# Performance work log

Measured on AMD Instinct MI355X. Metric: run time of the kernel, lower is better.

The kernel has to match this reference:

```python
import jax, jax.numpy as jnp
import numpy as np

N = 20000      # cells (nodes)
E = 640000     # kNN edges (before self loops)
IN = 2000      # gene features
C = 64         # out_channels
H = 4          # attention heads
NEG_SLOPE = 0.2
EPS = 1e-12


def setup_inputs() -> dict:
    key = jax.random.key(0)
    ks = jax.random.split(key, 12)
    s = lambda k, shape, sc: (jax.random.normal(k, shape, jnp.float32) * sc)
    x = s(ks[0], (N, IN), 1.0)
    edge_index = jax.random.randint(ks[1], (2, E), 0, N)
    W_ae = s(ks[2], (IN, C), 0.02); b_ae = jnp.zeros((C,), jnp.float32)
    Wl = s(ks[3], (C, H * C), 0.1); bl = jnp.zeros((H * C,), jnp.float32)
    Wr = s(ks[4], (C, H * C), 0.1); br = jnp.zeros((H * C,), jnp.float32)
    att = s(ks[5], (H, C), 0.1)
    b_conv = jnp.zeros((H * C,), jnp.float32)
    W_lin = s(ks[6], (H * C, C), 0.1); b_lin = jnp.zeros((C,), jnp.float32)
    ln_w = jnp.ones((C,), jnp.float32); ln_b = jnp.zeros((C,), jnp.float32)
    return dict(x=x, edge_index=edge_index, W_ae=W_ae, b_ae=b_ae, Wl=Wl, bl=bl,
                Wr=Wr, br=br, att=att, b_conv=b_conv, W_lin=W_lin, b_lin=b_lin,
                ln_w=ln_w, ln_b=ln_b)


def reference(x, edge_index, W_ae, b_ae, Wl, bl, Wr, br, att, b_conv,
              W_lin, b_lin, ln_w, ln_b):
    # Encoder.AE: linear projection of gene features -> node embeddings
    h = x @ W_ae + b_ae                              # [N, C]

    # GATv2Conv (PyG defaults: add_self_loops=True, negative_slope=0.2,
    # dropout is identity at eval, concat=True)
    loops = jnp.arange(N)
    src = jnp.concatenate([edge_index[0], loops])    # [E+N] message sources j
    dst = jnp.concatenate([edge_index[1], loops])    # [E+N] targets i

    xl = (h @ Wl + bl).reshape(N, H, C)              # W_l x (source features)
    xr = (h @ Wr + br).reshape(N, H, C)              # W_r x (target features)

    g = jax.nn.leaky_relu(xl[src] + xr[dst], NEG_SLOPE)   # [E+N, H, C]
    logits = jnp.einsum('ehc,hc->eh', g, att)             # [E+N, H]

    # segment softmax over incoming edges of each target node
    m = jax.ops.segment_max(logits, dst, num_segments=N)  # [N, H]
    e = jnp.exp(logits - m[dst])
    denom = jax.ops.segment_sum(e, dst, num_segments=N)   # [N, H] (>0: self loops)
    alpha = e / denom[dst]                                 # [E+N, H]

    out = jax.ops.segment_sum(alpha[:, :, None] * xl[src], dst, num_segments=N)
    out = out.reshape(N, H * C) + b_conv             # concat heads + bias

    # Encoder.linear + activation (relu), dropout = identity at eval
    a = jax.nn.relu(out @ W_lin + b_lin)             # [N, C]

    # residual + TF-style LayerNorm
    y = a + h
    u = y.mean(-1, keepdims=True)
    v = ((y - u) ** 2).mean(-1, keepdims=True)
    return ln_w * (y - u) / jnp.sqrt(v + EPS) + ln_b
```

## Files before the change

kernel.cpp:

```cpp
#include <hip/hip_runtime.h>
#include <hip/hip_fp16.h>

#define N_NODES 20000
#define N_EDGES 640000
#define IN_F    2000
#define KPAD    2048
#define C_OUT   64
#define HC      256
#define NEG     0.2f
#define SCAN_B  79

typedef __attribute__((ext_vector_type(4))) float f32x4;
typedef __attribute__((ext_vector_type(8))) short bf16x8;
typedef _Float16 h2 __attribute__((ext_vector_type(2)));

__device__ inline unsigned short f2bf(float f) {
    unsigned u = __float_as_uint(f);
    return (unsigned short)((u + 0x7FFFu + ((u >> 16) & 1u)) >> 16);
}


__global__ void k_hist(const int* __restrict__ dst, int* __restrict__ counts) {
    int e = blockIdx.x * blockDim.x + threadIdx.x;
    if (e < N_EDGES) atomicAdd(&counts[dst[e]], 1);
}

__global__ void k_scan1(const int* __restrict__ counts, int* __restrict__ bsum) {
    int t = threadIdx.x, b = blockIdx.x;
    int i = b * 256 + t;
    int v = (i < N_NODES) ? counts[i] : 0;
    int s = v;
    #pragma unroll
    for (int d = 1; d < 64; d <<= 1) s += __shfl_xor(s, d, 64);
    __shared__ int ws[4];
    if ((t & 63) == 0) ws[t >> 6] = s;
    __syncthreads();
    if (t == 0) bsum[b] = ws[0] + ws[1] + ws[2] + ws[3];
}

__global__ void k_scan2(const int* __restrict__ bsum, int* __restrict__ bbase,
                        int* __restrict__ offsets) {
    int lane = threadIdx.x;
    int v0 = (lane < SCAN_B) ? bsum[lane] : 0;
    int v1 = (64 + lane < SCAN_B) ? bsum[64 + lane] : 0;
    int s0 = v0;
    #pragma unroll
    for (int d = 1; d < 64; d <<= 1) { int t = __shfl_up(s0, d, 64); if (lane >= d) s0 += t; }
    int tot0 = __shfl(s0, 63, 64);
    int s1 = v1;
    #pragma unroll
    for (int d = 1; d < 64; d <<= 1) { int t = __shfl_up(s1, d, 64); if (lane >= d) s1 += t; }
    int tot1 = __shfl(s1, 63, 64);
    if (lane < SCAN_B) bbase[lane] = s0 - v0;
    if (64 + lane < SCAN_B) bbase[64 + lane] = tot0 + s1 - v1;
    if (lane == 0) offsets[N_NODES] = tot0 + tot1;
}

__global__ void k_scan3(const int* __restrict__ counts, const int* __restrict__ bbase,
                        int* __restrict__ offsets, int* __restrict__ cursor) {
    int t = threadIdx.x, b = blockIdx.x;
    int lane = t & 63, wid = t >> 6;
    int i = b * 256 + t;
    int v = (i < N_NODES) ? counts[i] : 0;
    int s = v;
    #pragma unroll
    for (int d = 1; d < 64; d <<= 1) { int u = __shfl_up(s, d, 64); if (lane >= d) s += u; }
    __shared__ int ws[4];
    if (lane == 63) ws[wid] = s;
    __syncthreads();
    int wb = 0;
    #pragma unroll
    for (int w = 0; w < 3; ++w) if (w < wid) wb += ws[w];
    int excl = bbase[b] + wb + (s - v);
    if (i < N_NODES) { offsets[i] = excl; cursor[i] = excl; }
}

__global__ void k_scatter(const int* __restrict__ src, const int* __restrict__ dst,
                          int* __restrict__ cursor, int* __restrict__ ssrc) {
    int e = blockIdx.x * blockDim.x + threadIdx.x;
    if (e < N_EDGES) {
        int d = dst[e];
        int p = atomicAdd(&cursor[d], 1);
        ssrc[p] = src[e];
    }
}


__global__ void k_wt(const float* __restrict__ W, unsigned short* __restrict__ Wt) {
    int idx = blockIdx.x * 256 + threadIdx.x;
    int n = idx >> 11;
    int k = idx & 2047;
    float v = (k < IN_F) ? W[(size_t)k * C_OUT + n] : 0.f;
    Wt[(size_t)n * KPAD + k] = f2bf(v);
}


__global__ __launch_bounds__(256) void k_gemm_h(
    const float* __restrict__ x, const unsigned short* __restrict__ Wt,
    const float* __restrict__ b, float* __restrict__ h) {
    __shared__ unsigned short Asw[32 * 64];
    __shared__ unsigned short Bsw[64 * 64];
    int t = threadIdx.x;
    int lane = t & 63, wid = t >> 6;
    int wr = wid >> 1, wc = wid & 1;
    int row0 = blockIdx.x * 32;

    int a_row = t & 31, a_half = t >> 5;
    int b_n = t >> 2, b_kq = t & 3;

    int rA = wr * 16 + (lane & 15);
    int kchunk = lane >> 4;
    f32x4 acc0 = {0.f, 0.f, 0.f, 0.f}, acc1 = {0.f, 0.f, 0.f, 0.f};

    for (int k0 = 0; k0 < KPAD; k0 += 64) {
        {
            uint4 wv = {0u, 0u, 0u, 0u};
            int kbase = k0 + a_half * 8;
            if (kbase < IN_F) {
                const float* src = &x[(size_t)(row0 + a_row) * IN_F + kbase];
                float4 f0 = *(const float4*)src;
                float4 f1 = *(const float4*)(src + 4);
                wv.x = (unsigned)f2bf(f0.x) | ((unsigned)f2bf(f0.y) << 16);
                wv.y = (unsigned)f2bf(f0.z) | ((unsigned)f2bf(f0.w) << 16);
                wv.z = (unsigned)f2bf(f1.x) | ((unsigned)f2bf(f1.y) << 16);
                wv.w = (unsigned)f2bf(f1.z) | ((unsigned)f2bf(f1.w) << 16);
            }
            int slot = a_half ^ (a_row & 7);
            *(uint4*)((char*)Asw + a_row * 128 + slot * 16) = wv;
        }
        {
            const uint4* src = (const uint4*)&Wt[(size_t)b_n * KPAD + k0 + b_kq * 16];
            uint4 w0 = src[0], w1 = src[1];
            int s0 = (b_kq * 2) ^ (b_n & 7);
            int s1 = (b_kq * 2 + 1) ^ (b_n & 7);
            *(uint4*)((char*)Bsw + b_n * 128 + s0 * 16) = w0;
            *(uint4*)((char*)Bsw + b_n * 128 + s1 * 16) = w1;
        }
        __syncthreads();
        #pragma unroll
        for (int ks = 0; ks < 2; ++ks) {
            int aslot = (ks * 4 + kchunk) ^ (rA & 7);
            bf16x8 af = *(bf16x8*)((char*)Asw + rA * 128 + aslot * 16);
            {
                int cb = wc * 32 + (lane & 15);
                int bslot = (ks * 4 + kchunk) ^ (cb & 7);
                bf16x8 bfr = *(bf16x8*)((char*)Bsw + cb * 128 + bslot * 16);
                acc0 = __builtin_amdgcn_mfma_f32_16x16x32_bf16(af, bfr, acc0, 0, 0, 0);
            }
            {
                int cb = wc * 32 + 16 + (lane & 15);
                int bslot = (ks * 4 + kchunk) ^ (cb & 7);
                bf16x8 bfr = *(bf16x8*)((char*)Bsw + cb * 128 + bslot * 16);
                acc1 = __builtin_amdgcn_mfma_f32_16x16x32_bf16(af, bfr, acc1, 0, 0, 0);
            }
        }
        __syncthreads();
    }
    int ci = (lane >> 4) * 4;
    int cj = lane & 15;
    #pragma unroll
    for (int nt = 0; nt < 2; ++nt) {
        f32x4 a = nt ? acc1 : acc0;
        int col = wc * 32 + nt * 16 + cj;
        float bb = b[col];
        #pragma unroll
        for (int r = 0; r < 4; ++r) {
            int grow = row0 + wr * 16 + ci + r;
            h[(size_t)grow * C_OUT + col] = a[r] + bb;
        }
    }
}


__global__ __launch_bounds__(256) void k_xlxr2(
    const float* __restrict__ h, const float* __restrict__ Wl, const float* __restrict__ bl,
    const float* __restrict__ Wr, const float* __restrict__ br,
    unsigned short* __restrict__ xlh, float* __restrict__ xr) {
    __shared__ float hs[64][68];
    __shared__ float Ws[64][128];
    int t = threadIdx.x;
    int mb = blockIdx.x >> 2, nb = blockIdx.x & 3;
    int node0 = mb * 64;
    const float* Wsrc = (nb < 2) ? (Wl + nb * 128) : (Wr + (nb - 2) * 128);
    const float* bsrc = (nb < 2) ? (bl + nb * 128) : (br + (nb - 2) * 128);

    {
        int row = t >> 2, q = t & 3;
        int gnode = node0 + row; if (gnode >= N_NODES) gnode = N_NODES - 1;
        const float4* src = (const float4*)&h[(size_t)gnode * C_OUT + q * 16];
        *(float4*)&hs[row][q * 16 + 0]  = src[0];
        *(float4*)&hs[row][q * 16 + 4]  = src[1];
        *(float4*)&hs[row][q * 16 + 8]  = src[2];
        *(float4*)&hs[row][q * 16 + 12] = src[3];
    }
    {
        #pragma unroll
        for (int i = 0; i < 8; ++i) {
            int f = t + i * 256;
            int k = f >> 5, c4 = (f & 31) << 2;
            *(float4*)&Ws[k][c4] = *(const float4*)&Wsrc[(size_t)k * HC + c4];
        }
    }
    __syncthreads();

    int tr = t >> 5;
    int tc = t & 31;
    float4 acc[8];
    float4 bv = *(const float4*)&bsrc[tc * 4];
    #pragma unroll
    for (int r = 0; r < 8; ++r) acc[r] = bv;

    for (int k4 = 0; k4 < 64; k4 += 4) {
        float4 w0 = *(float4*)&Ws[k4 + 0][tc * 4];
        float4 w1 = *(float4*)&Ws[k4 + 1][tc * 4];
        float4 w2 = *(float4*)&Ws[k4 + 2][tc * 4];
        float4 w3 = *(float4*)&Ws[k4 + 3][tc * 4];
        #pragma unroll
        for (int r = 0; r < 8; ++r) {
            float4 a = *(float4*)&hs[tr * 8 + r][k4];
            acc[r].x += a.x * w0.x + a.y * w1.x + a.z * w2.x + a.w * w3.x;
            acc[r].y += a.x * w0.y + a.y * w1.y + a.z * w2.y + a.w * w3.y;
            acc[r].z += a.x * w0.z + a.y * w1.z + a.z * w2.z + a.w * w3.z;
            acc[r].w += a.x * w0.w + a.y * w1.w + a.z * w2.w + a.w * w3.w;
        }
    }
    #pragma unroll
    for (int r = 0; r < 8; ++r) {
        int gnode = node0 + tr * 8 + r;
        if (gnode < N_NODES) {
            if (nb < 2) {
                h2 lo = { (_Float16)acc[r].x, (_Float16)acc[r].y };
                h2 hi = { (_Float16)acc[r].z, (_Float16)acc[r].w };
                uint2 o = { __builtin_bit_cast(unsigned, lo),
                            __builtin_bit_cast(unsigned, hi) };
                *(uint2*)&xlh[(size_t)gnode * HC + nb * 128 + tc * 4] = o;
            } else {
                *(float4*)&xr[(size_t)gnode * HC + (nb - 2) * 128 + tc * 4] = acc[r];
            }
        }
    }
}


__global__ __launch_bounds__(256) void k_attn(
    const unsigned short* __restrict__ xlh, const float* __restrict__ xr,
    const float* __restrict__ h, const int* __restrict__ offsets,
    const int* __restrict__ ssrc, const float* __restrict__ att,
    const float* __restrict__ b_conv, const float* __restrict__ W_lin,
    const float* __restrict__ b_lin, const float* __restrict__ ln_w,
    const float* __restrict__ ln_b, float* __restrict__ out) {
    __shared__ float sh[4][HC];
    int wid = threadIdx.x >> 6, lane = threadIdx.x & 63;
    int node = blockIdx.x * 4 + wid;
    int sub = lane >> 4;
    int sl  = lane & 15;
    int c0  = sl * 16;

    const h2 z2  = { (_Float16)0.f, (_Float16)0.f };
    const h2 ns2 = { (_Float16)NEG, (_Float16)NEG };

    h2 xr2[8], at2[8];
    #pragma unroll
    for (int i = 0; i < 4; ++i) {
        float4 t4 = *(const float4*)&xr[(size_t)node * HC + c0 + i * 4];
        xr2[i*2+0] = h2{ (_Float16)t4.x, (_Float16)t4.y };
        xr2[i*2+1] = h2{ (_Float16)t4.z, (_Float16)t4.w };
        float4 a4 = *(const float4*)&att[c0 + i * 4];
        at2[i*2+0] = h2{ (_Float16)a4.x, (_Float16)a4.y };
        at2[i*2+1] = h2{ (_Float16)a4.z, (_Float16)a4.w };
    }
    h2 acc2[8];
    #pragma unroll
    for (int i = 0; i < 8; ++i) acc2[i] = z2;
    float denom = 0.f;

    auto load_edge = [&](int j, uint4& w0, uint4& w1) {
        const uint4* rp = (const uint4*)&xlh[(size_t)j * HC + c0];
        w0 = rp[0]; w1 = rp[1];
    };
    auto compute_edge = [&](uint4 w0, uint4 w1, bool valid) {
        h2 x2[8];
        x2[0] = __builtin_bit_cast(h2, w0.x); x2[1] = __builtin_bit_cast(h2, w0.y);
        x2[2] = __builtin_bit_cast(h2, w0.z); x2[3] = __builtin_bit_cast(h2, w0.w);
        x2[4] = __builtin_bit_cast(h2, w1.x); x2[5] = __builtin_bit_cast(h2, w1.y);
        x2[6] = __builtin_bit_cast(h2, w1.z); x2[7] = __builtin_bit_cast(h2, w1.w);
        h2 p2 = z2;
        #pragma unroll
        for (int i = 0; i < 8; ++i) {
            h2 g  = x2[i] + xr2[i];
            h2 gs = g * ns2;
            g = __builtin_elementwise_max(g, gs);
            p2 += g * at2[i];
        }
        float p = (float)p2.x + (float)p2.y;
        p += __shfl_xor(p, 1); p += __shfl_xor(p, 2);
        float ex = valid ? __expf(p) : 0.f;
        denom += ex;
        h2 e2 = { (_Float16)ex, (_Float16)ex };
        #pragma unroll
        for (int i = 0; i < 8; ++i) acc2[i] += e2 * x2[i];
    };

    {
        uint4 s0v, s1v;
        load_edge(node, s0v, s1v);
        compute_edge(s0v, s1v, sub == 0);
    }

    int s0 = offsets[node], s1 = offsets[node + 1];
    for (int base = s0; base < s1; base += 64) {
        int rem = s1 - base;
        int cnt = rem < 64 ? rem : 64;
        int jv = (base + lane < s1) ? ssrc[base + lane] : 0;
        int niter = (cnt + 3) >> 2;
        uint4 a0, a1, b0, b1;
        int jA = __shfl(jv, sub, 64);
        load_edge(jA, a0, a1);
        for (int it = 0; it < niter; it += 2) {
            int eB = ((it + 1) << 2) + sub;
            int jB = __shfl(jv, eB & 63, 64);
            load_edge(jB, b0, b1);
            compute_edge(a0, a1, ((it << 2) + sub) < cnt);
            int eA2 = ((it + 2) << 2) + sub;
            int jA2 = __shfl(jv, eA2 & 63, 64);
            load_edge(jA2, a0, a1);
            compute_edge(b0, b1, eB < cnt);
        }
    }

    float accf[16];
    #pragma unroll
    for (int i = 0; i < 8; ++i) {
        accf[2*i]   = (float)acc2[i].x;
        accf[2*i+1] = (float)acc2[i].y;
    }
    #pragma unroll
    for (int i = 0; i < 16; ++i) {
        accf[i] += __shfl_xor(accf[i], 16);
        accf[i] += __shfl_xor(accf[i], 32);
    }
    denom += __shfl_xor(denom, 16);
    denom += __shfl_xor(denom, 32);

    float inv = 1.f / denom;
    if (sub == 0) {
        #pragma unroll
        for (int i = 0; i < 4; ++i) {
            float4 bc = *(const float4*)&b_conv[c0 + i * 4];
            float4 o = { accf[i*4+0] * inv + bc.x, accf[i*4+1] * inv + bc.y,
                         accf[i*4+2] * inv + bc.z, accf[i*4+3] * inv + bc.w };
            *(float4*)&sh[wid][c0 + i * 4] = o;
        }
    }
    __syncthreads();

    float s = b_lin[lane];
    #pragma unroll 8
    for (int k = 0; k < HC; k += 4) {
        float4 o4 = *(float4*)&sh[wid][k];
        s += o4.x * W_lin[(k + 0) * C_OUT + lane];
        s += o4.y * W_lin[(k + 1) * C_OUT + lane];
        s += o4.z * W_lin[(k + 2) * C_OUT + lane];
        s += o4.w * W_lin[(k + 3) * C_OUT + lane];
    }
    float a = s > 0.f ? s : 0.f;
    float y = a + h[(size_t)node * C_OUT + lane];

    float m = y;
    m += __shfl_xor(m, 1);  m += __shfl_xor(m, 2);  m += __shfl_xor(m, 4);
    m += __shfl_xor(m, 8);  m += __shfl_xor(m, 16); m += __shfl_xor(m, 32);
    m *= (1.f / 64.f);
    float d = y - m;
    float v2 = d * d;
    v2 += __shfl_xor(v2, 1);  v2 += __shfl_xor(v2, 2);  v2 += __shfl_xor(v2, 4);
    v2 += __shfl_xor(v2, 8);  v2 += __shfl_xor(v2, 16); v2 += __shfl_xor(v2, 32);
    v2 *= (1.f / 64.f);
    out[(size_t)node * C_OUT + lane] = ln_w[lane] * d * rsqrtf(v2 + 1e-12f) + ln_b[lane];
}


extern "C" void kernel_launch(void* const* d_in, const int* in_sizes, int n_in,
                              void* d_out, int out_size, void* d_ws, size_t ws_size,
                              hipStream_t stream) {
    const float* x     = (const float*)d_in[0];
    const int*   ei    = (const int*)  d_in[1];
    const float* W_ae  = (const float*)d_in[2];
    const float* b_ae  = (const float*)d_in[3];
    const float* Wl    = (const float*)d_in[4];
    const float* bl    = (const float*)d_in[5];
    const float* Wr    = (const float*)d_in[6];
    const float* br    = (const float*)d_in[7];
    const float* att   = (const float*)d_in[8];
    const float* b_conv= (const float*)d_in[9];
    const float* W_lin = (const float*)d_in[10];
    const float* b_lin = (const float*)d_in[11];
    const float* ln_w  = (const float*)d_in[12];
    const float* ln_b  = (const float*)d_in[13];
    float* out = (float*)d_out;
    const int* src = ei;
    const int* dst = ei + N_EDGES;

    char* ws = (char*)d_ws;
    size_t off = 0;
    auto alloc = [&](size_t bytes) {
        void* p = ws + off;
        off = (off + bytes + 255) & ~(size_t)255;
        return p;
    };
    float* h       = (float*)alloc((size_t)N_NODES * C_OUT * 4);
    unsigned short* xlh = (unsigned short*)alloc((size_t)N_NODES * HC * 2);
    float* xr      = (float*)alloc((size_t)N_NODES * HC * 4);
    int*   counts  = (int*)  alloc((size_t)N_NODES * 4);
    int*   offsets = (int*)  alloc((size_t)(N_NODES + 1) * 4);
    int*   cursor  = (int*)  alloc((size_t)N_NODES * 4);
    int*   ssrc    = (int*)  alloc((size_t)N_EDGES * 4);
    unsigned short* Wt = (unsigned short*)alloc((size_t)C_OUT * KPAD * 2);
    int*   bsum    = (int*)  alloc((size_t)SCAN_B * 4);
    int*   bbase   = (int*)  alloc((size_t)SCAN_B * 4);

    (void)hipMemsetAsync(counts, 0, (size_t)N_NODES * 4, stream);
    k_hist   <<<(N_EDGES + 255) / 256, 256, 0, stream>>>(dst, counts);
    k_scan1  <<<SCAN_B, 256, 0, stream>>>(counts, bsum);
    k_scan2  <<<1, 64, 0, stream>>>(bsum, bbase, offsets);
    k_scan3  <<<SCAN_B, 256, 0, stream>>>(counts, bbase, offsets, cursor);
    k_scatter<<<(N_EDGES + 255) / 256, 256, 0, stream>>>(src, dst, cursor, ssrc);
    k_wt     <<<(C_OUT * KPAD) / 256, 256, 0, stream>>>(W_ae, Wt);
    k_gemm_h <<<N_NODES / 32, 256, 0, stream>>>(x, Wt, b_ae, h);
    k_xlxr2  <<<((N_NODES + 63) / 64) * 4, 256, 0, stream>>>(h, Wl, bl, Wr, br, xlh, xr);
    k_attn   <<<N_NODES / 4, 256, 0, stream>>>(xlh, xr, h, offsets, ssrc, att,
                                               b_conv, W_lin, b_lin, ln_w, ln_b, out);
}
```

Baseline: 213.8 us.

## Split attention epilogue into MFMA post kernel and simplify h GEMM without LDS

The per-node W_lin matvec, ReLU, residual and LayerNorm move out of the attention kernel into a new k_post kernel. It runs an fp16 MFMA GEMM over attention outputs that are now staged as fp16 in a workspace buffer, using a transposed fp16 copy of W_lin. The attention kernel becomes one 64-thread block per node, with no shared memory and no block barrier. The x@W_ae GEMM also drops its LDS staging, and each wave now computes 16 rows by 64 columns, loading weights straight from global or cache. The cost is an extra 10MB round trip for the intermediate, two more launches, fp16 rounding of the conv output, and x rows read with less coalescing in the GEMM.

```diff
diff --git a/kernel.cpp b/kernel.cpp
--- a/kernel.cpp
+++ b/kernel.cpp
@@ -13,6 +13,7 @@
 typedef __attribute__((ext_vector_type(4))) float f32x4;
 typedef __attribute__((ext_vector_type(8))) short bf16x8;
 typedef _Float16 h2 __attribute__((ext_vector_type(2)));
+typedef _Float16 f16x8 __attribute__((ext_vector_type(8)));
 
 __device__ inline unsigned short f2bf(float f) {
     unsigned u = __float_as_uint(f);
@@ -94,79 +95,56 @@
     Wt[(size_t)n * KPAD + k] = f2bf(v);
 }
 
+__global__ void k_wlin16(const float* __restrict__ W, unsigned short* __restrict__ Wt16) {
+    int idx = blockIdx.x * 256 + threadIdx.x;
+    int col = idx >> 8;
+    int k = idx & 255;
+    _Float16 v = (_Float16)W[(size_t)k * C_OUT + col];
+    Wt16[(size_t)col * HC + k] = __builtin_bit_cast(unsigned short, v);
+}
+
 
 __global__ __launch_bounds__(256) void k_gemm_h(
     const float* __restrict__ x, const unsigned short* __restrict__ Wt,
     const float* __restrict__ b, float* __restrict__ h) {
-    __shared__ unsigned short Asw[32 * 64];
-    __shared__ unsigned short Bsw[64 * 64];
     int t = threadIdx.x;
-    int lane = t & 63, wid = t >> 6;
-    int wr = wid >> 1, wc = wid & 1;
-    int row0 = blockIdx.x * 32;
-
-    int a_row = t & 31, a_half = t >> 5;
-    int b_n = t >> 2, b_kq = t & 3;
-
-    int rA = wr * 16 + (lane & 15);
-    int kchunk = lane >> 4;
-    f32x4 acc0 = {0.f, 0.f, 0.f, 0.f}, acc1 = {0.f, 0.f, 0.f, 0.f};
-
-    for (int k0 = 0; k0 < KPAD; k0 += 64) {
-        {
-            uint4 wv = {0u, 0u, 0u, 0u};
-            int kbase = k0 + a_half * 8;
-            if (kbase < IN_F) {
-                const float* src = &x[(size_t)(row0 + a_row) * IN_F + kbase];
-                float4 f0 = *(const float4*)src;
-                float4 f1 = *(const float4*)(src + 4);
-                wv.x = (unsigned)f2bf(f0.x) | ((unsigned)f2bf(f0.y) << 16);
-                wv.y = (unsigned)f2bf(f0.z) | ((unsigned)f2bf(f0.w) << 16);
-                wv.z = (unsigned)f2bf(f1.x) | ((unsigned)f2bf(f1.y) << 16);
-                wv.w = (unsigned)f2bf(f1.z) | ((unsigned)f2bf(f1.w) << 16);
-            }
-            int slot = a_half ^ (a_row & 7);
-            *(uint4*)((char*)Asw + a_row * 128 + slot * 16) = wv;
-        }
-        {
-            const uint4* src = (const uint4*)&Wt[(size_t)b_n * KPAD + k0 + b_kq * 16];
-            uint4 w0 = src[0], w1 = src[1];
-            int s0 = (b_kq * 2) ^ (b_n & 7);
-            int s1 = (b_kq * 2 + 1) ^ (b_n & 7);
-            *(uint4*)((char*)Bsw + b_n * 128 + s0 * 16) = w0;
-            *(uint4*)((char*)Bsw + b_n * 128 + s1 * 16) = w1;
-        }
-        __syncthreads();
-        #pragma unroll
-        for (int ks = 0; ks < 2; ++ks) {
-            int aslot = (ks * 4 + kchunk) ^ (rA & 7);
-            bf16x8 af = *(bf16x8*)((char*)Asw + rA * 128 + aslot * 16);
-            {
-                int cb = wc * 32 + (lane & 15);
-                int bslot = (ks * 4 + kchunk) ^ (cb & 7);
-                bf16x8 bfr = *(bf16x8*)((char*)Bsw + cb * 128 + bslot * 16);
-                acc0 = __builtin_amdgcn_mfma_f32_16x16x32_bf16(af, bfr, acc0, 0, 0, 0);
-            }
-            {
-                int cb = wc * 32 + 16 + (lane & 15);
-                int bslot = (ks * 4 + kchunk) ^ (cb & 7);
-                bf16x8 bfr = *(bf16x8*)((char*)Bsw + cb * 128 + bslot * 16);
-                acc1 = __builtin_amdgcn_mfma_f32_16x16x32_bf16(af, bfr, acc1, 0, 0, 0);
-            }
-        }
-        __syncthreads();
-    }
-    int ci = (lane >> 4) * 4;
-    int cj = lane & 15;
-    #pragma unroll
-    for (int nt = 0; nt < 2; ++nt) {
-        f32x4 a = nt ? acc1 : acc0;
-        int col = wc * 32 + nt * 16 + cj;
+    int lane = t & 63, w = t >> 6;
+    int row0 = blockIdx.x * 64 + w * 16;
+    int r = lane & 15, kc = lane >> 4;
+    int row = row0 + r;
+    int rowc = row < N_NODES ? row : N_NODES - 1;
+    const float* xrow = x + (size_t)rowc * IN_F;
+    f32x4 acc[4] = {{0,0,0,0},{0,0,0,0},{0,0,0,0},{0,0,0,0}};
+
+    for (int k0 = 0; k0 < 2016; k0 += 32) {
+        int kb = k0 + kc * 8;
+        bf16x8 af = {0,0,0,0,0,0,0,0};
+        if (kb < IN_F) {
+            float4 f0 = *(const float4*)&xrow[kb];
+            float4 f1 = *(const float4*)&xrow[kb + 4];
+            uint4 uu;
+            uu.x = (unsigned)f2bf(f0.x) | ((unsigned)f2bf(f0.y) << 16);
+            uu.y = (unsigned)f2bf(f0.z) | ((unsigned)f2bf(f0.w) << 16);
+            uu.z = (unsigned)f2bf(f1.x) | ((unsigned)f2bf(f1.y) << 16);
+            uu.w = (unsigned)f2bf(f1.z) | ((unsigned)f2bf(f1.w) << 16);
+            af = __builtin_bit_cast(bf16x8, uu);
+        }
+        #pragma unroll
+        for (int cb = 0; cb < 4; ++cb) {
+            bf16x8 bf = *(const bf16x8*)&Wt[(size_t)(cb * 16 + r) * KPAD + kb];
+            acc[cb] = __builtin_amdgcn_mfma_f32_16x16x32_bf16(af, bf, acc[cb], 0, 0, 0);
+        }
+    }
+    int ci = (lane >> 4) * 4, cj = lane & 15;
+    #pragma unroll
+    for (int cb = 0; cb < 4; ++cb) {
+        int col = cb * 16 + cj;
         float bb = b[col];
         #pragma unroll
-        for (int r = 0; r < 4; ++r) {
-            int grow = row0 + wr * 16 + ci + r;
-            h[(size_t)grow * C_OUT + col] = a[r] + bb;
+        for (int rr = 0; rr < 4; ++rr) {
+            int grow = row0 + ci + rr;
+            if (grow < N_NODES)
+                h[(size_t)grow * C_OUT + col] = acc[cb][rr] + bb;
         }
     }
 }
@@ -242,16 +220,13 @@
 }
 
 
-__global__ __launch_bounds__(256) void k_attn(
+__global__ __launch_bounds__(64) void k_attn(
     const unsigned short* __restrict__ xlh, const float* __restrict__ xr,
-    const float* __restrict__ h, const int* __restrict__ offsets,
-    const int* __restrict__ ssrc, const float* __restrict__ att,
-    const float* __restrict__ b_conv, const float* __restrict__ W_lin,
-    const float* __restrict__ b_lin, const float* __restrict__ ln_w,
-    const float* __restrict__ ln_b, float* __restrict__ out) {
-    __shared__ float sh[4][HC];
-    int wid = threadIdx.x >> 6, lane = threadIdx.x & 63;
-    int node = blockIdx.x * 4 + wid;
+    const int* __restrict__ offsets, const int* __restrict__ ssrc,
+    const float* __restrict__ att, const float* __restrict__ b_conv,
+    unsigned short* __restrict__ ovh) {
+    int lane = threadIdx.x;
+    int node = blockIdx.x;
     int sub = lane >> 4;
     int sl  = lane & 15;
     int c0  = sl * 16;
@@ -344,38 +319,85 @@
 
     float inv = 1.f / denom;
     if (sub == 0) {
+        float bcf[16];
         #pragma unroll
         for (int i = 0; i < 4; ++i) {
             float4 bc = *(const float4*)&b_conv[c0 + i * 4];
-            float4 o = { accf[i*4+0] * inv + bc.x, accf[i*4+1] * inv + bc.y,
-                         accf[i*4+2] * inv + bc.z, accf[i*4+3] * inv + bc.w };
-            *(float4*)&sh[wid][c0 + i * 4] = o;
-        }
-    }
-    __syncthreads();
-
-    float s = b_lin[lane];
-    #pragma unroll 8
-    for (int k = 0; k < HC; k += 4) {
-        float4 o4 = *(float4*)&sh[wid][k];
-        s += o4.x * W_lin[(k + 0) * C_OUT + lane];
-        s += o4.y * W_lin[(k + 1) * C_OUT + lane];
-        s += o4.z * W_lin[(k + 2) * C_OUT + lane];
-        s += o4.w * W_lin[(k + 3) * C_OUT + lane];
-    }
-    float a = s > 0.f ? s : 0.f;
-    float y = a + h[(size_t)node * C_OUT + lane];
-
-    float m = y;
-    m += __shfl_xor(m, 1);  m += __shfl_xor(m, 2);  m += __shfl_xor(m, 4);
-    m += __shfl_xor(m, 8);  m += __shfl_xor(m, 16); m += __shfl_xor(m, 32);
-    m *= (1.f / 64.f);
-    float d = y - m;
-    float v2 = d * d;
-    v2 += __shfl_xor(v2, 1);  v2 += __shfl_xor(v2, 2);  v2 += __shfl_xor(v2, 4);
-    v2 += __shfl_xor(v2, 8);  v2 += __shfl_xor(v2, 16); v2 += __shfl_xor(v2, 32);
-    v2 *= (1.f / 64.f);
-    out[(size_t)node * C_OUT + lane] = ln_w[lane] * d * rsqrtf(v2 + 1e-12f) + ln_b[lane];
+            bcf[i*4+0] = bc.x; bcf[i*4+1] = bc.y; bcf[i*4+2] = bc.z; bcf[i*4+3] = bc.w;
+        }
+        unsigned ww[8];
+        #pragma unroll
+        for (int i = 0; i < 8; ++i) {
+            h2 p = { (_Float16)(accf[2*i]   * inv + bcf[2*i]),
+                     (_Float16)(accf[2*i+1] * inv + bcf[2*i+1]) };
+            ww[i] = __builtin_bit_cast(unsigned, p);
+        }
+        uint4 o0 = { ww[0], ww[1], ww[2], ww[3] };
+        uint4 o1 = { ww[4], ww[5], ww[6], ww[7] };
+        *(uint4*)&ovh[(size_t)node * HC + c0]     = o0;
+        *(uint4*)&ovh[(size_t)node * HC + c0 + 8] = o1;
+    }
+}
+
+
+__global__ __launch_bounds__(256) void k_post(
+    const unsigned short* __restrict__ ovh, const unsigned short* __restrict__ Wt16,
+    const float* __restrict__ b_lin, const float* __restrict__ hbuf,
+    const float* __restrict__ ln_w, const float* __restrict__ ln_b,
+    float* __restrict__ out) {
+    int t = threadIdx.x;
+    int lane = t & 63, w = t >> 6;
+    int node0 = blockIdx.x * 64 + w * 16;
+    int r = lane & 15, kc = lane >> 4;
+    int noder = node0 + r;
+    int nodec = noder < N_NODES ? noder : N_NODES - 1;
+
+    f32x4 acc[4] = {{0,0,0,0},{0,0,0,0},{0,0,0,0},{0,0,0,0}};
+    #pragma unroll
+    for (int k0 = 0; k0 < HC; k0 += 32) {
+        int kb = k0 + kc * 8;
+        f16x8 af = *(const f16x8*)&ovh[(size_t)nodec * HC + kb];
+        #pragma unroll
+        for (int cb = 0; cb < 4; ++cb) {
+            f16x8 bf = *(const f16x8*)&Wt16[(size_t)(cb * 16 + r) * HC + kb];
+            acc[cb] = __builtin_amdgcn_mfma_f32_16x16x32_f16(af, bf, acc[cb], 0, 0, 0);
+        }
+    }
+
+    int ci = (lane >> 4) * 4, cj = lane & 15;
+    #pragma unroll
+    for (int rr = 0; rr < 4; ++rr) {
+        int grow = node0 + ci + rr;
+        int growc = grow < N_NODES ? grow : N_NODES - 1;
+        float y[4];
+        float ssum = 0.f;
+        #pragma unroll
+        for (int cb = 0; cb < 4; ++cb) {
+            int col = cb * 16 + cj;
+            float a = acc[cb][rr] + b_lin[col];
+            a = a > 0.f ? a : 0.f;
+            float yy = a + hbuf[(size_t)growc * C_OUT + col];
+            y[cb] = yy;
+            ssum += yy;
+        }
+        ssum += __shfl_xor(ssum, 1); ssum += __shfl_xor(ssum, 2);
+        ssum += __shfl_xor(ssum, 4); ssum += __shfl_xor(ssum, 8);
+        float m = ssum * (1.f / 64.f);
+        float vs = 0.f;
+        #pragma unroll
+        for (int cb = 0; cb < 4; ++cb) { float d = y[cb] - m; vs += d * d; }
+        vs += __shfl_xor(vs, 1); vs += __shfl_xor(vs, 2);
+        vs += __shfl_xor(vs, 4); vs += __shfl_xor(vs, 8);
+        float rinv = rsqrtf(vs * (1.f / 64.f) + 1e-12f);
+        if (grow < N_NODES) {
+            #pragma unroll
+            for (int cb = 0; cb < 4; ++cb) {
+                int col = cb * 16 + cj;
+                out[(size_t)grow * C_OUT + col] =
+                    ln_w[col] * (y[cb] - m) * rinv + ln_b[col];
+            }
+        }
+    }
 }
 
 
@@ -410,11 +432,13 @@
     float* h       = (float*)alloc((size_t)N_NODES * C_OUT * 4);
     unsigned short* xlh = (unsigned short*)alloc((size_t)N_NODES * HC * 2);
     float* xr      = (float*)alloc((size_t)N_NODES * HC * 4);
+    unsigned short* ovh = (unsigned short*)alloc((size_t)N_NODES * HC * 2);
     int*   counts  = (int*)  alloc((size_t)N_NODES * 4);
     int*   offsets = (int*)  alloc((size_t)(N_NODES + 1) * 4);
     int*   cursor  = (int*)  alloc((size_t)N_NODES * 4);
     int*   ssrc    = (int*)  alloc((size_t)N_EDGES * 4);
-    unsigned short* Wt = (unsigned short*)alloc((size_t)C_OUT * KPAD * 2);
+    unsigned short* Wt   = (unsigned short*)alloc((size_t)C_OUT * KPAD * 2);
+    unsigned short* Wt16 = (unsigned short*)alloc((size_t)C_OUT * HC * 2);
     int*   bsum    = (int*)  alloc((size_t)SCAN_B * 4);
     int*   bbase   = (int*)  alloc((size_t)SCAN_B * 4);
 
@@ -425,8 +449,10 @@
     k_scan3  <<<SCAN_B, 256, 0, stream>>>(counts, bbase, offsets, cursor);
     k_scatter<<<(N_EDGES + 255) / 256, 256, 0, stream>>>(src, dst, cursor, ssrc);
     k_wt     <<<(C_OUT * KPAD) / 256, 256, 0, stream>>>(W_ae, Wt);
-    k_gemm_h <<<N_NODES / 32, 256, 0, stream>>>(x, Wt, b_ae, h);
+    k_wlin16 <<<(C_OUT * HC) / 256, 256, 0, stream>>>(W_lin, Wt16);
+    k_gemm_h <<<(N_NODES + 63) / 64, 256, 0, stream>>>(x, Wt, b_ae, h);
     k_xlxr2  <<<((N_NODES + 63) / 64) * 4, 256, 0, stream>>>(h, Wl, bl, Wr, br, xlh, xr);
-    k_attn   <<<N_NODES / 4, 256, 0, stream>>>(xlh, xr, h, offsets, ssrc, att,
-                                               b_conv, W_lin, b_lin, ln_w, ln_b, out);
-}
+    k_attn   <<<N_NODES, 64, 0, stream>>>(xlh, xr, offsets, ssrc, att, b_conv, ovh);
+    k_post   <<<(N_NODES + 63) / 64, 256, 0, stream>>>(ovh, Wt16, b_lin, h,
+                                                       ln_w, ln_b, out);
+}
```

Measured after the change: 245.1 us. +14.7%, slower.
